# Kernel tuning notes

Measured on AMD Instinct MI355X. Metric: run time of the kernel, lower is better.

The kernel has to match this reference:

```python
import jax, jax.numpy as jnp
import numpy as np
import math

B, D_MODEL, EMB, ORDER, SEQ = 4, 64, 33, 64, 256
TARGET, FAST_PCT, SLOW_PCT = 0.01, 0.3, 1.5


def _pos_emb(L, emb_dim):
    # PositionalEmbedding: t in [0,1], complex exponential bands
    t = jnp.linspace(0.0, 1.0, L)[None, :, None]                     # [1,L,1]
    bands = (emb_dim - 1) // 2
    t_r = jnp.linspace(0.0, L - 1.0, L)[None, :, None]
    w = 2.0 * math.pi * t_r / L
    f = jnp.linspace(1e-4, bands - 1.0, bands)[None, None]
    zc = jnp.exp(-1j * f * w)
    z = jnp.concatenate([t, zc.real, zc.imag], axis=-1)              # [1,L,emb_dim]
    return z.astype(jnp.float32), t.astype(jnp.float32)


def setup_inputs() -> dict:
    key = jax.random.key(0)
    ks = jax.random.split(key, 24)
    z, _ = _pos_emb(SEQ, EMB)

    def lin(k, fan_in, fan_out):
        return jax.random.normal(k, (fan_in, fan_out), jnp.float32) / np.sqrt(fan_in)

    inp = {
        'x': jax.random.normal(ks[0], (B, D_MODEL, SEQ, SEQ), jnp.float32),
        'z': z,
        'Xw1': lin(ks[1], EMB, ORDER), 'Xb1': jax.random.normal(ks[2], (ORDER,), jnp.float32) * 0.02,
        'Xw2': lin(ks[3], ORDER, ORDER), 'Xb2': jax.random.normal(ks[4], (ORDER,), jnp.float32) * 0.02,
        'Xw3': lin(ks[5], ORDER, ORDER), 'Xb3': jax.random.normal(ks[6], (ORDER,), jnp.float32) * 0.02,
        'Xwo': lin(ks[7], ORDER, D_MODEL),
        'Xfreq': jnp.ones((1, ORDER), jnp.float32),  # Sin freq, w=1, shared across layers
        'Yw1': lin(ks[8], EMB, ORDER), 'Yb1': jax.random.normal(ks[9], (ORDER,), jnp.float32) * 0.02,
        'Yw2': lin(ks[10], ORDER, ORDER), 'Yb2': jax.random.normal(ks[11], (ORDER,), jnp.float32) * 0.02,
        'Yw3': lin(ks[12], ORDER, ORDER), 'Yb3': jax.random.normal(ks[13], (ORDER,), jnp.float32) * 0.02,
        'Ywo': lin(ks[14], ORDER, D_MODEL),
        'Yfreq': jnp.ones((1, ORDER), jnp.float32),
        'bias': jax.random.normal(ks[15], (D_MODEL,), jnp.float32),
        'L': SEQ,
    }
    return inp


def _implicit_filter(z, w1, b1, w2, b2, w3, b3, wo, freq, t, deltas):
    # MLP with shared Sin activation, then exponential modulation (shift=0)
    h = jnp.sin(freq * (z @ w1 + b1))
    h = jnp.sin(freq * (h @ w2 + b2))
    h = jnp.sin(freq * (h @ w3 + b3))
    h = h @ wo                                   # [1,L,d_model]
    decay = jnp.exp(-t * jnp.abs(deltas))        # [1,L,d_model]
    return h * decay


def reference(x, z, Xw1, Xb1, Xw2, Xb2, Xw3, Xb3, Xwo, Xfreq,
              Yw1, Yb1, Yw2, Yb2, Yw3, Yb3, Ywo, Yfreq, bias, L):
    d_model = x.shape[1]
    t = jnp.linspace(0.0, 1.0, L)[None, :, None].astype(jnp.float32)
    max_dec = math.log(TARGET) / FAST_PCT
    min_dec = math.log(TARGET) / SLOW_PCT
    deltas = jnp.linspace(min_dec, max_dec, d_model)[None, None].astype(jnp.float32)

    hx = _implicit_filter(z, Xw1, Xb1, Xw2, Xb2, Xw3, Xb3, Xwo, Xfreq, t, deltas)
    hy = _implicit_filter(z, Yw1, Yb1, Yw2, Yb2, Yw3, Yb3, Ywo, Yfreq, t, deltas)
    # separable outer-product 2D kernel: [1,L,L,d_model] -> [d_model,L,L]
    k = jnp.einsum('ijk,imk->ijmk', hx, hy)[0]
    k = jnp.transpose(k, (2, 0, 1))

    fft_size = 2 * L
    k_f = jnp.fft.rfft2(k, s=(fft_size, fft_size)) / fft_size       # [D, 2L, L+1]
    u_f = jnp.fft.rfft2(x.astype(jnp.float32), s=(fft_size, fft_size))  # [B, D, 2L, L+1]
    y = jnp.fft.irfft2(u_f * k_f, s=(fft_size, fft_size))[..., :L, :L]
    out = y + x * bias[:, None, None]
    return out.astype(x.dtype)
```

## Files before the change

kernel.cpp:

```cpp
#include <hip/hip_runtime.h>

#define SL 256
#define RSTRIDE 312

typedef _Float16 f16;
typedef _Float16 f16x8 __attribute__((ext_vector_type(8)));
typedef _Float16 f16x4 __attribute__((ext_vector_type(4)));
typedef float f32x4 __attribute__((ext_vector_type(4)));

__global__ __launch_bounds__(64) void k_filters(
    const float* __restrict__ z,
    const float* __restrict__ Xw1, const float* __restrict__ Xb1,
    const float* __restrict__ Xw2, const float* __restrict__ Xb2,
    const float* __restrict__ Xw3, const float* __restrict__ Xb3,
    const float* __restrict__ Xwo, const float* __restrict__ Xfreq,
    const float* __restrict__ Yw1, const float* __restrict__ Yb1,
    const float* __restrict__ Yw2, const float* __restrict__ Yb2,
    const float* __restrict__ Yw3, const float* __restrict__ Yb3,
    const float* __restrict__ Ywo, const float* __restrict__ Yfreq,
    f16* __restrict__ hxT, f16* __restrict__ hyT)
{
    const int l = blockIdx.x;
    const int sel = blockIdx.y;
    const int t = threadIdx.x;
    const float* w1 = sel ? Yw1 : Xw1;  const float* b1 = sel ? Yb1 : Xb1;
    const float* w2 = sel ? Yw2 : Xw2;  const float* b2 = sel ? Yb2 : Xb2;
    const float* w3 = sel ? Yw3 : Xw3;  const float* b3 = sel ? Yb3 : Xb3;
    const float* wo = sel ? Ywo : Xwo;  const float* freq = sel ? Yfreq : Xfreq;
    f16* hT = sel ? hyT : hxT;

    __shared__ float zb[33];
    __shared__ float ha[64];
    __shared__ float hb[64];

    if (t < 33) zb[t] = z[l * 33 + t];
    __syncthreads();

    const float fr = freq[t];
    float s = b1[t];
    for (int k = 0; k < 33; ++k) s += zb[k] * w1[k * 64 + t];
    ha[t] = sinf(fr * s);
    __syncthreads();

    s = b2[t];
    for (int k = 0; k < 64; ++k) s += ha[k] * w2[k * 64 + t];
    hb[t] = sinf(fr * s);
    __syncthreads();

    s = b3[t];
    for (int k = 0; k < 64; ++k) s += hb[k] * w3[k * 64 + t];
    ha[t] = sinf(fr * s);
    __syncthreads();

    s = 0.f;
    for (int k = 0; k < 64; ++k) s += ha[k] * wo[k * 64 + t];

    const float MIN_DEC = -3.0701134573253937f;
    const float MAX_DEC = -15.350567286626968f;
    float ad = fabsf(MIN_DEC + (MAX_DEC - MIN_DEC) * ((float)t / 63.0f));
    float tl = (float)l / 255.0f;
    hT[t * 256 + l] = (f16)(s * expf(-tl * ad));
}

__device__ __forceinline__ f16x8 cvt8(float4 a, float4 b)
{
    f16x8 h;
    h[0] = (f16)a.x; h[1] = (f16)a.y; h[2] = (f16)a.z; h[3] = (f16)a.w;
    h[4] = (f16)b.x; h[5] = (f16)b.y; h[6] = (f16)b.z; h[7] = (f16)b.w;
    return h;
}

template<int NT>
__device__ __forceinline__ void build_R(f16* R, const f16* __restrict__ hc,
                                        int tid)
{
    for (int idx = tid; idx < 8 * RSTRIDE; idx += NT) {
        int c = idx / RSTRIDE;
        int k = idx - c * RSTRIDE;
        int u = k + c;
        R[idx] = (u <= 255) ? hc[255 - u] : (f16)0.f;
    }
}

__device__ __forceinline__ void bar_lgkm()
{
    asm volatile("s_waitcnt lgkmcnt(0)" ::: "memory");
    __builtin_amdgcn_s_barrier();
    __builtin_amdgcn_sched_barrier(0);
}

template<int JC>
__device__ __forceinline__ void p1_work(
    const f16x8* axs, const f16* __restrict__ Ry, f16* __restrict__ buf,
    int wave, int ln, int quad)
{
    f32x4 acc[8];
#pragma unroll
    for (int t = 0; t < 8; ++t) acc[t] = (f32x4){0.f, 0.f, 0.f, 0.f};

#pragma unroll
    for (int s = 0; s <= 4 * JC + 3; ++s) {
        const int q0 = s * 32;
#pragma unroll
        for (int c8 = 0; c8 < 8; ++c8) {
            if (s <= 4 * JC + (c8 >> 1)) {
                const int j = JC * 128 + c8 * 16 + ln;
                const int s0 = 255 - j + q0 + quad * 8;
                const int c = s0 & 7;
                f16x8 bf = *(const f16x8*)&Ry[c * RSTRIDE + (s0 - c)];
                acc[c8] = __builtin_amdgcn_mfma_f32_16x16x32_f16(
                    axs[s], bf, acc[c8], 0, 0, 0);
            }
        }
    }
#pragma unroll
    for (int c8 = 0; c8 < 8; ++c8) {
        const int jl = c8 * 16 + ln;
        const int pb = wave * 16 + quad * 4;
        f32x4 a = acc[c8];
        f16x4 v;
        v[0] = (f16)a[0]; v[1] = (f16)a[1];
        v[2] = (f16)a[2]; v[3] = (f16)a[3];
        *(f16x4*)&buf[jl * 256 + (pb ^ ((jl & 7) << 3))] = v;
    }
}

template<int JC>
__device__ __forceinline__ void p2_chunk(
    const f16* __restrict__ buf, const f16* __restrict__ Rx,
    const float* __restrict__ xbd, float* __restrict__ obd, float bv,
    int igrp, int jgrp, int ln, int quad)
{
    f32x4 acc[8];
#pragma unroll
    for (int t = 0; t < 8; ++t) acc[t] = (f32x4){0.f, 0.f, 0.f, 0.f};

    const int nst = igrp + 1;
    for (int s = 0; s < nst; ++s) {
        const int p0 = s * 32;
        f16x8 af[4];
#pragma unroll
        for (int jt = 0; jt < 4; ++jt) {
            const int jl = jgrp * 64 + jt * 16 + ln;
            const int off = (p0 + quad * 8) ^ ((jl & 7) << 3);
            af[jt] = *(const f16x8*)&buf[jl * 256 + off];
        }
#pragma unroll
        for (int ct = 0; ct < 2; ++ct) {
            const int i = igrp * 32 + ct * 16 + ln;
            const int s0 = 255 - i + p0 + quad * 8;
            const int c = s0 & 7;
            f16x8 bf = *(const f16x8*)&Rx[c * RSTRIDE + (s0 - c)];
#pragma unroll
            for (int jt = 0; jt < 4; ++jt)
                acc[ct * 4 + jt] = __builtin_amdgcn_mfma_f32_16x16x32_f16(
                    af[jt], bf, acc[ct * 4 + jt], 0, 0, 0);
        }
    }

    const float sc = 1.0f / 512.0f;
#pragma unroll
    for (int ct = 0; ct < 2; ++ct) {
        const int i = igrp * 32 + ct * 16 + ln;
#pragma unroll
        for (int jt = 0; jt < 4; ++jt) {
            const int j = JC * 128 + jgrp * 64 + jt * 16 + quad * 4;
            f32x4 a = acc[ct * 4 + jt];
            float4 xv = *(const float4*)(xbd + i * SL + j);
            float4 o;
            o.x = a[0] * sc + xv.x * bv;
            o.y = a[1] * sc + xv.y * bv;
            o.z = a[2] * sc + xv.z * bv;
            o.w = a[3] * sc + xv.w * bv;
            *(float4*)(obd + i * SL + j) = o;
        }
    }
}

__global__ __launch_bounds__(1024, 4) void k_pipe(
    const float* __restrict__ x, const f16* __restrict__ hxT,
    const f16* __restrict__ hyT, const float* __restrict__ bias,
    float* __restrict__ out)
{
    extern __shared__ __align__(16) f16 smem[];
    f16* buf0 = smem;
    f16* buf1 = smem + 128 * 256;
    f16* Ry   = smem + 2 * 128 * 256;
    f16* Rx   = Ry + 8 * RSTRIDE;

    const int bd = blockIdx.x;
    const int d  = bd & 63;
    const int tid  = threadIdx.x;
    const int lane = tid & 63;
    const int wave = tid >> 6;
    const int ln   = lane & 15;
    const int quad = lane >> 4;
    const int igrp = wave >> 1;
    const int jgrp = wave & 1;

    const float* xbd = x + (size_t)bd * (SL * SL);
    float* obd = out + (size_t)bd * (SL * SL);

    build_R<1024>(Ry, hyT + d * 256, tid);
    build_R<1024>(Rx, hxT + d * 256, tid);

    const float* xr = xbd + (wave * 16 + ln) * SL + quad * 8;
    const float bv = bias[d];

    float4 q[16];
#pragma unroll
    for (int s = 0; s < 8; ++s) {
        q[2 * s]     = *(const float4*)(xr + s * 32);
        q[2 * s + 1] = *(const float4*)(xr + s * 32 + 4);
    }
    __builtin_amdgcn_sched_barrier(0);

    f16x8 axs[8];
#pragma unroll
    for (int s = 0; s < 4; ++s)
        axs[s] = cvt8(q[2 * s], q[2 * s + 1]);

    bar_lgkm();

    p1_work<0>(axs, Ry, buf0, wave, ln, quad);

    bar_lgkm();

    p2_chunk<0>(buf0, Rx, xbd, obd, bv, igrp, jgrp, ln, quad);

#pragma unroll
    for (int s = 4; s < 8; ++s)
        axs[s] = cvt8(q[2 * s], q[2 * s + 1]);

    p1_work<1>(axs, Ry, buf1, wave, ln, quad);

    bar_lgkm();

    p2_chunk<1>(buf1, Rx, xbd, obd, bv, igrp, jgrp, ln, quad);
}

template<int J0>
__device__ __forceinline__ void phase1(
    const float* __restrict__ xr0, const float* __restrict__ xr1,
    const f16* __restrict__ R, f32x4 (&acc)[16], int ln, int quad)
{
    constexpr int QS = (J0 == 0) ? 4 : 8;
    float4 a0 = *(const float4*)xr0;
    float4 a1 = *(const float4*)(xr0 + 4);
    float4 b0 = *(const float4*)xr1;
    float4 b1 = *(const float4*)(xr1 + 4);

#pragma unroll
    for (int s = 0; s < QS; ++s) {
        const int q0 = s * 32;
        f16x8 af0 = cvt8(a0, a1);
        f16x8 af1 = cvt8(b0, b1);
        if (s + 1 < QS) {
            a0 = *(const float4*)(xr0 + q0 + 32);
            a1 = *(const float4*)(xr0 + q0 + 36);
            b0 = *(const float4*)(xr1 + q0 + 32);
            b1 = *(const float4*)(xr1 + q0 + 36);
        }
#pragma unroll
        for (int c8 = 0; c8 < 8; ++c8) {
            if (32 * s <= J0 + c8 * 16 + 15) {
                int j = J0 + c8 * 16 + ln;
                int s0 = 255 - j + q0 + quad * 8;
                int c = s0 & 7;
                f16x8 bf = *(const f16x8*)&R[c * RSTRIDE + (s0 - c)];
                acc[c8] = __builtin_amdgcn_mfma_f32_16x16x32_f16(
                    af0, bf, acc[c8], 0, 0, 0);
                acc[8 + c8] = __builtin_amdgcn_mfma_f32_16x16x32_f16(
                    af1, bf, acc[8 + c8], 0, 0, 0);
            }
        }
    }
}

__global__ __launch_bounds__(512, 4) void k_fused(
    const float* __restrict__ x, const f16* __restrict__ hxT,
    const f16* __restrict__ hyT, const float* __restrict__ bias,
    float* __restrict__ out)
{
    const int bd = blockIdx.x & 255;
    const int j0 = (blockIdx.x >> 8) << 7;
    const int d  = bd & 63;
    const int tid  = threadIdx.x;
    const int lane = tid & 63;
    const int wave = tid >> 6;
    const int ln   = lane & 15;
    const int quad = lane >> 4;

    __shared__ __align__(16) f16 tmp[128 * 256];
    __shared__ __align__(16) f16 R[8 * RSTRIDE];

    const float* xbd = x + (size_t)bd * (SL * SL);

    build_R<512>(R, hyT + d * 256, tid);

    f32x4 acc[16];
#pragma unroll
    for (int a = 0; a < 16; ++a) acc[a] = (f32x4){0.f, 0.f, 0.f, 0.f};

    __syncthreads();

    {
        const float* xr0 = xbd + (wave * 32 + ln) * SL + quad * 8;
        const float* xr1 = xr0 + 16 * SL;
        if (j0 == 0) phase1<0>(xr0, xr1, R, acc, ln, quad);
        else         phase1<128>(xr0, xr1, R, acc, ln, quad);

#pragma unroll
        for (int r = 0; r < 2; ++r)
#pragma unroll
            for (int c8 = 0; c8 < 8; ++c8) {
                int jl = c8 * 16 + ln;
                int pb = wave * 32 + r * 16 + quad * 4;
                f32x4 a = acc[r * 8 + c8];
                f16x4 v;
                v[0] = (f16)a[0]; v[1] = (f16)a[1];
                v[2] = (f16)a[2]; v[3] = (f16)a[3];
                *(f16x4*)&tmp[jl * 256 + (pb ^ ((jl & 7) << 3))] = v;
            }
    }

    __syncthreads();
    build_R<512>(R, hxT + d * 256, tid);
#pragma unroll
    for (int a = 0; a < 16; ++a) acc[a] = (f32x4){0.f, 0.f, 0.f, 0.f};
    __syncthreads();

    const int igrp = wave & 3;
    const int jgrp = wave >> 2;
    const int nst = (igrp + 1) * 2;
    for (int s = 0; s < nst; ++s) {
        const int p0 = s * 32;
        f16x8 af[4];
#pragma unroll
        for (int rt = 0; rt < 4; ++rt) {
            int jl = jgrp * 64 + rt * 16 + ln;
            int off = (p0 + quad * 8) ^ ((jl & 7) << 3);
            af[rt] = *(const f16x8*)&tmp[jl * 256 + off];
        }
#pragma unroll
        for (int ct = 0; ct < 4; ++ct) {
            if (p0 <= igrp * 64 + ct * 16 + 15) {
                int i = igrp * 64 + ct * 16 + ln;
                int s0 = 255 - i + p0 + quad * 8;
                int c = s0 & 7;
                f16x8 bf = *(const f16x8*)&R[c * RSTRIDE + (s0 - c)];
#pragma unroll
                for (int rt = 0; rt < 4; ++rt)
                    acc[rt * 4 + ct] = __builtin_amdgcn_mfma_f32_16x16x32_f16(
                        af[rt], bf, acc[rt * 4 + ct], 0, 0, 0);
            }
        }
    }

    const float bv = bias[d];
    const float sc = 1.0f / 512.0f;
    float* obd = out + (size_t)bd * (SL * SL);
#pragma unroll
    for (int rt = 0; rt < 4; ++rt)
#pragma unroll
        for (int ct = 0; ct < 4; ++ct) {
            int i = igrp * 64 + ct * 16 + ln;
            int j = j0 + jgrp * 64 + rt * 16 + quad * 4;
            f32x4 a = acc[rt * 4 + ct];
            float4 xv = *(const float4*)(xbd + i * SL + j);
            float4 o;
            o.x = a[0] * sc + xv.x * bv;
            o.y = a[1] * sc + xv.y * bv;
            o.z = a[2] * sc + xv.z * bv;
            o.w = a[3] * sc + xv.w * bv;
            *(float4*)(obd + i * SL + j) = o;
        }
}

extern "C" void kernel_launch(void* const* d_in, const int* in_sizes, int n_in,
                              void* d_out, int out_size, void* d_ws, size_t ws_size,
                              hipStream_t stream)
{
    (void)in_sizes; (void)n_in; (void)out_size; (void)ws_size;
    const float* x     = (const float*)d_in[0];
    const float* z     = (const float*)d_in[1];
    const float* Xw1   = (const float*)d_in[2];
    const float* Xb1   = (const float*)d_in[3];
    const float* Xw2   = (const float*)d_in[4];
    const float* Xb2   = (const float*)d_in[5];
    const float* Xw3   = (const float*)d_in[6];
    const float* Xb3   = (const float*)d_in[7];
    const float* Xwo   = (const float*)d_in[8];
    const float* Xfreq = (const float*)d_in[9];
    const float* Yw1   = (const float*)d_in[10];
    const float* Yb1   = (const float*)d_in[11];
    const float* Yw2   = (const float*)d_in[12];
    const float* Yb2   = (const float*)d_in[13];
    const float* Yw3   = (const float*)d_in[14];
    const float* Yb3   = (const float*)d_in[15];
    const float* Ywo   = (const float*)d_in[16];
    const float* Yfreq = (const float*)d_in[17];
    const float* bias  = (const float*)d_in[18];

    f16* hxT = (f16*)d_ws;
    f16* hyT = hxT + 64 * 256;

    k_filters<<<dim3(256, 2), 64, 0, stream>>>(
        z, Xw1, Xb1, Xw2, Xb2, Xw3, Xb3, Xwo, Xfreq,
        Yw1, Yb1, Yw2, Yb2, Yw3, Yb3, Ywo, Yfreq, hxT, hyT);

    const int dyn_lds = (2 * 128 * 256 + 2 * 8 * RSTRIDE) * (int)sizeof(f16);
    static hipError_t attr_rc = hipFuncSetAttribute(
        (const void*)k_pipe, hipFuncAttributeMaxDynamicSharedMemorySize, dyn_lds);

    if (attr_rc == hipSuccess) {
        k_pipe<<<256, 1024, dyn_lds, stream>>>(x, hxT, hyT, bias, (float*)d_out);
    } else {
        k_fused<<<512, 512, 0, stream>>>(x, hxT, hyT, bias, (float*)d_out);
    }
}
```

Before: 164.4 us.

## Split column pipeline into four 64-wide chunks with smaller ping-pong buffers

The two-phase causal-convolution pipeline in k_pipe now runs over four 64-column chunks instead of two 128-column chunks. Each wave computes one 16-row tile in the second phase rather than a 32x64 tile. The intermediate LDS buffers shrink by half, which cuts shared-memory footprint and accumulator registers and adds more pipeline stages for overlap. The cost is more barriers and less register reuse of the A fragments in the second phase, and the first phase loads less work per wave per stage.

```diff
diff --git a/kernel.cpp b/kernel.cpp
--- a/kernel.cpp
+++ b/kernel.cpp
@@ -90,34 +90,34 @@
 }
 
 template<int JC>
-__device__ __forceinline__ void p1_work(
+__device__ __forceinline__ void p1c(
     const f16x8* axs, const f16* __restrict__ Ry, f16* __restrict__ buf,
     int wave, int ln, int quad)
 {
-    f32x4 acc[8];
-#pragma unroll
-    for (int t = 0; t < 8; ++t) acc[t] = (f32x4){0.f, 0.f, 0.f, 0.f};
-
-#pragma unroll
-    for (int s = 0; s <= 4 * JC + 3; ++s) {
+    f32x4 acc[4];
+#pragma unroll
+    for (int t = 0; t < 4; ++t) acc[t] = (f32x4){0.f, 0.f, 0.f, 0.f};
+
+#pragma unroll
+    for (int s = 0; s <= 2 * JC + 1; ++s) {
         const int q0 = s * 32;
 #pragma unroll
-        for (int c8 = 0; c8 < 8; ++c8) {
-            if (s <= 4 * JC + (c8 >> 1)) {
-                const int j = JC * 128 + c8 * 16 + ln;
+        for (int c4 = 0; c4 < 4; ++c4) {
+            if (s <= 2 * JC + (c4 >> 1)) {
+                const int j = JC * 64 + c4 * 16 + ln;
                 const int s0 = 255 - j + q0 + quad * 8;
                 const int c = s0 & 7;
                 f16x8 bf = *(const f16x8*)&Ry[c * RSTRIDE + (s0 - c)];
-                acc[c8] = __builtin_amdgcn_mfma_f32_16x16x32_f16(
-                    axs[s], bf, acc[c8], 0, 0, 0);
+                acc[c4] = __builtin_amdgcn_mfma_f32_16x16x32_f16(
+                    axs[s], bf, acc[c4], 0, 0, 0);
             }
         }
     }
 #pragma unroll
-    for (int c8 = 0; c8 < 8; ++c8) {
-        const int jl = c8 * 16 + ln;
+    for (int c4 = 0; c4 < 4; ++c4) {
+        const int jl = c4 * 16 + ln;
         const int pb = wave * 16 + quad * 4;
-        f32x4 a = acc[c8];
+        f32x4 a = acc[c4];
         f16x4 v;
         v[0] = (f16)a[0]; v[1] = (f16)a[1];
         v[2] = (f16)a[2]; v[3] = (f16)a[3];
@@ -126,54 +126,44 @@
 }
 
 template<int JC>
-__device__ __forceinline__ void p2_chunk(
+__device__ __forceinline__ void p2c(
     const f16* __restrict__ buf, const f16* __restrict__ Rx,
     const float* __restrict__ xbd, float* __restrict__ obd, float bv,
-    int igrp, int jgrp, int ln, int quad)
-{
-    f32x4 acc[8];
-#pragma unroll
-    for (int t = 0; t < 8; ++t) acc[t] = (f32x4){0.f, 0.f, 0.f, 0.f};
-
-    const int nst = igrp + 1;
+    int t, int ln, int quad)
+{
+    f32x4 acc[4];
+#pragma unroll
+    for (int a = 0; a < 4; ++a) acc[a] = (f32x4){0.f, 0.f, 0.f, 0.f};
+
+    const int nst = (t >> 1) + 1;
+    const int i = t * 16 + ln;
     for (int s = 0; s < nst; ++s) {
         const int p0 = s * 32;
-        f16x8 af[4];
+        const int s0 = 255 - i + p0 + quad * 8;
+        const int c = s0 & 7;
+        f16x8 bf = *(const f16x8*)&Rx[c * RSTRIDE + (s0 - c)];
 #pragma unroll
         for (int jt = 0; jt < 4; ++jt) {
-            const int jl = jgrp * 64 + jt * 16 + ln;
+            const int jl = jt * 16 + ln;
             const int off = (p0 + quad * 8) ^ ((jl & 7) << 3);
-            af[jt] = *(const f16x8*)&buf[jl * 256 + off];
-        }
-#pragma unroll
-        for (int ct = 0; ct < 2; ++ct) {
-            const int i = igrp * 32 + ct * 16 + ln;
-            const int s0 = 255 - i + p0 + quad * 8;
-            const int c = s0 & 7;
-            f16x8 bf = *(const f16x8*)&Rx[c * RSTRIDE + (s0 - c)];
-#pragma unroll
-            for (int jt = 0; jt < 4; ++jt)
-                acc[ct * 4 + jt] = __builtin_amdgcn_mfma_f32_16x16x32_f16(
-                    af[jt], bf, acc[ct * 4 + jt], 0, 0, 0);
+            f16x8 af = *(const f16x8*)&buf[jl * 256 + off];
+            acc[jt] = __builtin_amdgcn_mfma_f32_16x16x32_f16(
+                af, bf, acc[jt], 0, 0, 0);
         }
     }
 
     const float sc = 1.0f / 512.0f;
 #pragma unroll
-    for (int ct = 0; ct < 2; ++ct) {
-        const int i = igrp * 32 + ct * 16 + ln;
-#pragma unroll
-        for (int jt = 0; jt < 4; ++jt) {
-            const int j = JC * 128 + jgrp * 64 + jt * 16 + quad * 4;
-            f32x4 a = acc[ct * 4 + jt];
-            float4 xv = *(const float4*)(xbd + i * SL + j);
-            float4 o;
-            o.x = a[0] * sc + xv.x * bv;
-            o.y = a[1] * sc + xv.y * bv;
-            o.z = a[2] * sc + xv.z * bv;
-            o.w = a[3] * sc + xv.w * bv;
-            *(float4*)(obd + i * SL + j) = o;
-        }
+    for (int jt = 0; jt < 4; ++jt) {
+        const int j = JC * 64 + jt * 16 + quad * 4;
+        f32x4 a = acc[jt];
+        float4 xv = *(const float4*)(xbd + i * SL + j);
+        float4 o;
+        o.x = a[0] * sc + xv.x * bv;
+        o.y = a[1] * sc + xv.y * bv;
+        o.z = a[2] * sc + xv.z * bv;
+        o.w = a[3] * sc + xv.w * bv;
+        *(float4*)(obd + i * SL + j) = o;
     }
 }
 
@@ -184,8 +174,8 @@
 {
     extern __shared__ __align__(16) f16 smem[];
     f16* buf0 = smem;
-    f16* buf1 = smem + 128 * 256;
-    f16* Ry   = smem + 2 * 128 * 256;
+    f16* buf1 = smem + 64 * 256;
+    f16* Ry   = smem + 2 * 64 * 256;
     f16* Rx   = Ry + 8 * RSTRIDE;
 
     const int bd = blockIdx.x;
@@ -195,8 +185,6 @@
     const int wave = tid >> 6;
     const int ln   = lane & 15;
     const int quad = lane >> 4;
-    const int igrp = wave >> 1;
-    const int jgrp = wave & 1;
 
     const float* xbd = x + (size_t)bd * (SL * SL);
     float* obd = out + (size_t)bd * (SL * SL);
@@ -216,27 +204,32 @@
     __builtin_amdgcn_sched_barrier(0);
 
     f16x8 axs[8];
-#pragma unroll
-    for (int s = 0; s < 4; ++s)
-        axs[s] = cvt8(q[2 * s], q[2 * s + 1]);
+    axs[0] = cvt8(q[0], q[1]);
+    axs[1] = cvt8(q[2], q[3]);
 
     bar_lgkm();
-
-    p1_work<0>(axs, Ry, buf0, wave, ln, quad);
+    p1c<0>(axs, Ry, buf0, wave, ln, quad);
+    axs[2] = cvt8(q[4], q[5]);
+    axs[3] = cvt8(q[6], q[7]);
 
     bar_lgkm();
-
-    p2_chunk<0>(buf0, Rx, xbd, obd, bv, igrp, jgrp, ln, quad);
-
-#pragma unroll
-    for (int s = 4; s < 8; ++s)
-        axs[s] = cvt8(q[2 * s], q[2 * s + 1]);
-
-    p1_work<1>(axs, Ry, buf1, wave, ln, quad);
+    p2c<0>(buf0, Rx, xbd, obd, bv, wave, ln, quad);
+    p1c<1>(axs, Ry, buf1, wave, ln, quad);
+    axs[4] = cvt8(q[8], q[9]);
+    axs[5] = cvt8(q[10], q[11]);
 
     bar_lgkm();
-
-    p2_chunk<1>(buf1, Rx, xbd, obd, bv, igrp, jgrp, ln, quad);
+    p2c<1>(buf1, Rx, xbd, obd, bv, wave, ln, quad);
+    p1c<2>(axs, Ry, buf0, wave, ln, quad);
+    axs[6] = cvt8(q[12], q[13]);
+    axs[7] = cvt8(q[14], q[15]);
+
+    bar_lgkm();
+    p2c<2>(buf0, Rx, xbd, obd, bv, wave, ln, quad);
+    p1c<3>(axs, Ry, buf1, wave, ln, quad);
+
+    bar_lgkm();
+    p2c<3>(buf1, Rx, xbd, obd, bv, wave, ln, quad);
 }
 
 template<int J0>
@@ -409,7 +402,7 @@
         z, Xw1, Xb1, Xw2, Xb2, Xw3, Xb3, Xwo, Xfreq,
         Yw1, Yb1, Yw2, Yb2, Yw3, Yb3, Ywo, Yfreq, hxT, hyT);
 
-    const int dyn_lds = (2 * 128 * 256 + 2 * 8 * RSTRIDE) * (int)sizeof(f16);
+    const int dyn_lds = (2 * 64 * 256 + 2 * 8 * RSTRIDE) * (int)sizeof(f16);
     static hipError_t attr_rc = hipFuncSetAttribute(
         (const void*)k_pipe, hipFuncAttributeMaxDynamicSharedMemorySize, dyn_lds);
 
```

Measured after the change: 166.3 us. Within noise of the previous version (+1.2%).
